# Optimization experiments

Hardware: AMD Instinct MI355X
Metric: run time of the kernel (lower is better)

## Reference

```python
import jax, jax.numpy as jnp
import numpy as np

NUM_NODES = 100000
NUM_EDGES = 1600000
NUM_GRAPHS = 512
HIDDEN = 128
LAYERS = 3
NUM_CLASSES = 10
BN_EPS = 1e-5


def setup_inputs() -> dict:
    key = jax.random.key(0)
    ks = jax.random.split(key, 12)
    x = jax.random.normal(ks[0], (NUM_NODES, HIDDEN), dtype=jnp.float32)
    edge_index = jax.random.randint(ks[1], (2, NUM_EDGES), 0, NUM_NODES, dtype=jnp.int32)
    batch = jnp.sort(jax.random.randint(ks[2], (NUM_NODES,), 0, NUM_GRAPHS, dtype=jnp.int32))
    s = 1.0 / np.sqrt(HIDDEN)
    W1 = jax.random.normal(ks[3], (LAYERS, HIDDEN, HIDDEN), dtype=jnp.float32) * s
    b1 = jnp.zeros((LAYERS, HIDDEN), dtype=jnp.float32)
    W2 = jax.random.normal(ks[4], (LAYERS, HIDDEN, HIDDEN), dtype=jnp.float32) * s
    b2 = jnp.zeros((LAYERS, HIDDEN), dtype=jnp.float32)
    gamma = jnp.ones((LAYERS, HIDDEN), dtype=jnp.float32)
    beta = jnp.zeros((LAYERS, HIDDEN), dtype=jnp.float32)
    eps_gin = jnp.zeros((LAYERS,), dtype=jnp.float32)  # train_eps init 0
    lin1_w = jax.random.normal(ks[5], (LAYERS * HIDDEN, HIDDEN), dtype=jnp.float32) * (1.0 / np.sqrt(LAYERS * HIDDEN))
    lin1_b = jnp.zeros((HIDDEN,), dtype=jnp.float32)
    lin2_w = jax.random.normal(ks[6], (HIDDEN, NUM_CLASSES), dtype=jnp.float32) * s
    lin2_b = jnp.zeros((NUM_CLASSES,), dtype=jnp.float32)
    return {"x": x, "edge_index": edge_index, "batch": batch,
            "W1": W1, "b1": b1, "W2": W2, "b2": b2,
            "gamma": gamma, "beta": beta, "eps_gin": eps_gin,
            "lin1_w": lin1_w, "lin1_b": lin1_b, "lin2_w": lin2_w, "lin2_b": lin2_b}


def _batchnorm(h, g, b):
    mu = jnp.mean(h, axis=0, keepdims=True)
    var = jnp.var(h, axis=0, keepdims=True)
    return (h - mu) * jax.lax.rsqrt(var + BN_EPS) * g + b


def reference(x, edge_index, batch, W1, b1, W2, b2, gamma, beta, eps_gin,
              lin1_w, lin1_b, lin2_w, lin2_b):
    src, dst = edge_index[0], edge_index[1]
    n = x.shape[0]
    h = x
    layer_hs = []
    for l in range(LAYERS):
        # scatter-add neighbor aggregation: agg[i] = sum_{j->i} h[j]
        agg = jax.ops.segment_sum(h[src], dst, num_segments=n)
        z = (1.0 + eps_gin[l]) * h + agg
        z = jax.nn.relu(z @ W1[l] + b1[l])
        z = jax.nn.relu(z @ W2[l] + b2[l])
        h = _batchnorm(z, gamma[l], beta[l])
        layer_hs.append(h)
    h_cat = jnp.concatenate(layer_hs, axis=-1)  # [N, LAYERS*HIDDEN]
    # global mean pool per graph
    sums = jax.ops.segment_sum(h_cat, batch, num_segments=NUM_GRAPHS)
    counts = jax.ops.segment_sum(jnp.ones((n, 1), h_cat.dtype), batch, num_segments=NUM_GRAPHS)
    g = sums / jnp.maximum(counts, 1.0)
    g = jax.nn.relu(g @ lin1_w + lin1_b)
    # dropout is identity in inference
    return g @ lin2_w + lin2_b
```

## Files before the change

### kernel.cpp

```cpp
#include <hip/hip_runtime.h>

#define HID 128
#define NGRAPH 512
#define NLAYERS 3
#define BN_EPS 1e-5f
#define NPB 256
#define EB 4096

typedef __attribute__((ext_vector_type(8))) short bf16x8;
typedef __attribute__((ext_vector_type(4))) float f32x4;
typedef __attribute__((ext_vector_type(2))) float f32x2;

__device__ inline unsigned short f2bf(float x) {
    union { float f; unsigned u; } v; v.f = x;
    unsigned r = v.u + 0x7FFFu + ((v.u >> 16) & 1u);
    return (unsigned short)(r >> 16);
}
__device__ inline float bf2f(unsigned short b) {
    union { float f; unsigned u; } v; v.u = ((unsigned)b) << 16; return v.f;
}
__device__ inline f32x2 bfp(unsigned u) {
    union { unsigned q; float f; } lo, hi;
    lo.q = u << 16; hi.q = u & 0xFFFF0000u;
    f32x2 r; r[0] = lo.f; r[1] = hi.f; return r;
}

__global__ void k_prep(const float4* __restrict__ x4, ushort* __restrict__ xb, int total4,
                       const float* __restrict__ W1, ushort* __restrict__ w1h, ushort* __restrict__ w1l,
                       const float* __restrict__ W2, ushort* __restrict__ w2h, ushort* __restrict__ w2l,
                       int wtotal, int xblocks,
                       const int* __restrict__ dst, int E, int* __restrict__ blkcnt,
                       int* __restrict__ btot) {
    __shared__ int hist[512];
    int b = blockIdx.x, t = threadIdx.x;
    if (b < 384) {
        int gid = b * 256 + t;
        const float* W; ushort *Wh, *Wl; int e;
        if (gid < wtotal) { W = W1; Wh = w1h; Wl = w1l; e = gid; }
        else              { W = W2; Wh = w2h; Wl = w2l; e = gid - wtotal; }
        if (e < wtotal) {
            int l = e >> 14, rem = e & 16383, k = rem >> 7, n = rem & 127;
            float v = W[e];
            ushort hi = f2bf(v);
            ushort lo = f2bf(v - bf2f(hi));
            int o = (l << 14) + (n << 7) + k;
            Wh[o] = hi; Wl[o] = lo;
        }
    } else if (b < 384 + xblocks) {
        int i = (b - 384) * 256 + t;
        if (i < total4) {
            float4 v = x4[i];
            uint2 p;
            p.x = ((unsigned)f2bf(v.y) << 16) | f2bf(v.x);
            p.y = ((unsigned)f2bf(v.w) << 16) | f2bf(v.z);
            ((uint2*)xb)[i] = p;
        }
    } else {
        int b2 = b - (384 + xblocks);
        hist[t] = 0; hist[t + 256] = 0;
        __syncthreads();
        int base = b2 * EB;
        #pragma unroll
        for (int i = 0; i < 16; ++i) {
            int e = base + i * 256 + t;
            if (e < E) atomicAdd(&hist[dst[e] >> 8], 1);
        }
        __syncthreads();
        blkcnt[b2 * 512 + t]       = hist[t];
        blkcnt[b2 * 512 + t + 256] = hist[t + 256];
        if (hist[t])       atomicAdd(&btot[t], hist[t]);
        if (hist[t + 256]) atomicAdd(&btot[t + 256], hist[t + 256]);
    }
}

__global__ __launch_bounds__(512) void k_bscan(const int* __restrict__ tot, int nb, int E,
                                               int* __restrict__ bbase, int* __restrict__ rowptrN) {
    __shared__ int sh[512];
    int t = threadIdx.x;
    sh[t] = (t < nb) ? tot[t] : 0;
    __syncthreads();
    #pragma unroll
    for (int s = 1; s < 512; s <<= 1) {
        int v = (t >= s) ? sh[t - s] : 0;
        __syncthreads();
        sh[t] += v;
        __syncthreads();
    }
    if (t < nb) bbase[t] = (t == 0) ? 0 : sh[t - 1];
    if (t == 0) { bbase[nb] = E; *rowptrN = E; }
}

__global__ __launch_bounds__(512) void k_colscan(int* __restrict__ blkcnt, int eblk,
                                                 const int* __restrict__ bbase) {
    __shared__ int sh[512];
    int t = threadIdx.x;
    int b = blockIdx.x;
    sh[t] = (t < eblk) ? blkcnt[t * 512 + b] : 0;
    __syncthreads();
    #pragma unroll
    for (int s = 1; s < 512; s <<= 1) {
        int v = (t >= s) ? sh[t - s] : 0;
        __syncthreads();
        sh[t] += v;
        __syncthreads();
    }
    int excl = (t == 0) ? 0 : sh[t - 1];
    if (t < eblk) blkcnt[t * 512 + b] = bbase[b] + excl;
}

__global__ __launch_bounds__(256) void k_bscatter(const int* __restrict__ src,
                                                  const int* __restrict__ dst, int E,
                                                  const int* __restrict__ blkcnt,
                                                  unsigned* __restrict__ pairs) {
    __shared__ int hist[512];
    __shared__ int lbase[512];
    int t = threadIdx.x;
    hist[t] = 0; hist[t + 256] = 0;
    lbase[t]       = blkcnt[blockIdx.x * 512 + t];
    lbase[t + 256] = blkcnt[blockIdx.x * 512 + t + 256];
    __syncthreads();
    int base = blockIdx.x * EB;
    #pragma unroll
    for (int i = 0; i < 16; ++i) {
        int e = base + i * 256 + t;
        if (e < E) {
            int d = dst[e];
            int b = d >> 8;
            int pos = lbase[b] + atomicAdd(&hist[b], 1);
            pairs[pos] = ((unsigned)(d & 255) << 24) | (unsigned)src[e];
        }
    }
}

__global__ __launch_bounds__(256) void k_bbuild(const unsigned* __restrict__ pairs,
                                                const int* __restrict__ bbase, int N,
                                                int* __restrict__ rowptr, int* __restrict__ csr) {
    __shared__ int cnt[256];
    __shared__ int off[256];
    int t = threadIdx.x;
    int b = blockIdx.x;
    int base = bbase[b], bcount = bbase[b + 1] - base;
    cnt[t] = 0;
    __syncthreads();
    for (int i = t; i < bcount; i += 256) atomicAdd(&cnt[pairs[base + i] >> 24], 1);
    __syncthreads();
    off[t] = cnt[t];
    __syncthreads();
    for (int s = 1; s < 256; s <<= 1) {
        int v = (t >= s) ? off[t - s] : 0;
        __syncthreads();
        off[t] += v;
        __syncthreads();
    }
    int excl = (t == 0) ? 0 : off[t - 1];
    int node = b * NPB + t;
    if (node < N) rowptr[node] = base + excl;
    cnt[t] = excl;
    __syncthreads();
    for (int i = t; i < bcount; i += 256) {
        unsigned p = pairs[base + i];
        int dl = p >> 24;
        int pos = base + atomicAdd(&cnt[dl], 1);
        csr[pos] = (int)(p & 0xFFFFFFu);
    }
}

__global__ __launch_bounds__(256, 6) void k_agg(
        const int* __restrict__ rowptr, const int* __restrict__ csr_src,
        const uint2* __restrict__ hinb,
        const float* __restrict__ prev_sliced,
        const float* __restrict__ g_row, const float* __restrict__ be_row,
        const float* __restrict__ eps_gin, int layer,
        ushort* __restrict__ z0out, int N) {
    __shared__ float sfold[256];
    const int t = threadIdx.x;
    const int lane = t & 63;
    const int wv = t >> 6;
    const int q = lane >> 4;
    const int f = lane & 15;

    if (prev_sliced) {
        float s = 0.f;
        #pragma unroll
        for (int k = 0; k < 8; ++k) s += prev_sliced[k * 768 + t];
        sfold[t] = s;
        __syncthreads();
    }

    f32x2 scv2[4], shv2[4];
    if (prev_sliced) {
        float invn = 1.0f / (float)N;
        #pragma unroll
        for (int d = 0; d < 4; ++d) {
            #pragma unroll
            for (int h = 0; h < 2; ++h) {
                int fi = f * 8 + d * 2 + h;
                float mu = sfold[fi] * invn;
                float var = sfold[128 + fi] * invn - mu * mu;
                float inv = rsqrtf(var + BN_EPS);
                float scj = g_row[fi] * inv;
                scv2[d][h] = scj; shv2[d][h] = be_row[fi] - mu * scj;
            }
        }
    } else {
        #pragma unroll
        for (int d = 0; d < 4; ++d) { scv2[d] = (f32x2){1.f, 1.f}; shv2[d] = (f32x2){0.f, 0.f}; }
    }
    float e1 = 1.0f + eps_gin[layer];
    const uint4* hin4 = (const uint4*)hinb;

    int r = blockIdx.x * 16 + wv * 4 + q;
    f32x2 a2[4];
    #pragma unroll
    for (int d = 0; d < 4; ++d) a2[d] = (f32x2){0.f, 0.f};
    float cdeg = 0.f;
    if (r < N) {
        int beg = rowptr[r], end = rowptr[r + 1];
        uint4 hv = hin4[(size_t)r * 16 + f];
        a2[0] = e1 * bfp(hv.x); a2[1] = e1 * bfp(hv.y);
        a2[2] = e1 * bfp(hv.z); a2[3] = e1 * bfp(hv.w);
        int p = beg;
        for (; p + 8 <= end; p += 8) {
            int s0 = csr_src[p],     s1 = csr_src[p + 1], s2 = csr_src[p + 2], s3 = csr_src[p + 3];
            int s4 = csr_src[p + 4], s5 = csr_src[p + 5], s6 = csr_src[p + 6], s7 = csr_src[p + 7];
            uint4 v0 = hin4[(size_t)s0 * 16 + f];
            uint4 v1 = hin4[(size_t)s1 * 16 + f];
            uint4 v2 = hin4[(size_t)s2 * 16 + f];
            uint4 v3 = hin4[(size_t)s3 * 16 + f];
            uint4 v4 = hin4[(size_t)s4 * 16 + f];
            uint4 v5 = hin4[(size_t)s5 * 16 + f];
            uint4 v6 = hin4[(size_t)s6 * 16 + f];
            uint4 v7 = hin4[(size_t)s7 * 16 + f];
            a2[0] += ((bfp(v0.x) + bfp(v1.x)) + (bfp(v2.x) + bfp(v3.x)))
                   + ((bfp(v4.x) + bfp(v5.x)) + (bfp(v6.x) + bfp(v7.x)));
            a2[1] += ((bfp(v0.y) + bfp(v1.y)) + (bfp(v2.y) + bfp(v3.y)))
                   + ((bfp(v4.y) + bfp(v5.y)) + (bfp(v6.y) + bfp(v7.y)));
            a2[2] += ((bfp(v0.z) + bfp(v1.z)) + (bfp(v2.z) + bfp(v3.z)))
                   + ((bfp(v4.z) + bfp(v5.z)) + (bfp(v6.z) + bfp(v7.z)));
            a2[3] += ((bfp(v0.w) + bfp(v1.w)) + (bfp(v2.w) + bfp(v3.w)))
                   + ((bfp(v4.w) + bfp(v5.w)) + (bfp(v6.w) + bfp(v7.w)));
        }
        if (p < end) {
            int last = end - 1;
            int c1 = min(p + 1, last), c2 = min(p + 2, last), c3 = min(p + 3, last);
            int c4 = min(p + 4, last), c5 = min(p + 5, last), c6 = min(p + 6, last);
            int s0 = csr_src[p],  s1 = csr_src[c1], s2 = csr_src[c2], s3 = csr_src[c3];
            int s4 = csr_src[c4], s5 = csr_src[c5], s6 = csr_src[c6];
            uint4 v0 = hin4[(size_t)s0 * 16 + f];
            uint4 v1 = hin4[(size_t)s1 * 16 + f];
            uint4 v2 = hin4[(size_t)s2 * 16 + f];
            uint4 v3 = hin4[(size_t)s3 * 16 + f];
            uint4 v4 = hin4[(size_t)s4 * 16 + f];
            uint4 v5 = hin4[(size_t)s5 * 16 + f];
            uint4 v6 = hin4[(size_t)s6 * 16 + f];
            int rem = end - p;
            unsigned m1 = (rem > 1) ? 0xFFFFFFFFu : 0u;
            unsigned m2 = (rem > 2) ? 0xFFFFFFFFu : 0u;
            unsigned m3 = (rem > 3) ? 0xFFFFFFFFu : 0u;
            unsigned m4 = (rem > 4) ? 0xFFFFFFFFu : 0u;
            unsigned m5 = (rem > 5) ? 0xFFFFFFFFu : 0u;
            unsigned m6 = (rem > 6) ? 0xFFFFFFFFu : 0u;
            a2[0] += ((bfp(v0.x) + bfp(v1.x & m1)) + (bfp(v2.x & m2) + bfp(v3.x & m3)))
                   + ((bfp(v4.x & m4) + bfp(v5.x & m5)) + bfp(v6.x & m6));
            a2[1] += ((bfp(v0.y) + bfp(v1.y & m1)) + (bfp(v2.y & m2) + bfp(v3.y & m3)))
                   + ((bfp(v4.y & m4) + bfp(v5.y & m5)) + bfp(v6.y & m6));
            a2[2] += ((bfp(v0.z) + bfp(v1.z & m1)) + (bfp(v2.z & m2) + bfp(v3.z & m3)))
                   + ((bfp(v4.z & m4) + bfp(v5.z & m5)) + bfp(v6.z & m6));
            a2[3] += ((bfp(v0.w) + bfp(v1.w & m1)) + (bfp(v2.w & m2) + bfp(v3.w & m3)))
                   + ((bfp(v4.w & m4) + bfp(v5.w & m5)) + bfp(v6.w & m6));
        }
        cdeg = e1 + (float)(end - beg);
    }
    f32x2 rr2[4];
    #pragma unroll
    for (int d = 0; d < 4; ++d) rr2[d] = scv2[d] * a2[d] + cdeg * shv2[d];
    uint4 ph;
    ph.x = ((unsigned)f2bf(rr2[0][1]) << 16) | f2bf(rr2[0][0]);
    ph.y = ((unsigned)f2bf(rr2[1][1]) << 16) | f2bf(rr2[1][0]);
    ph.z = ((unsigned)f2bf(rr2[2][1]) << 16) | f2bf(rr2[2][0]);
    ph.w = ((unsigned)f2bf(rr2[3][1]) << 16) | f2bf(rr2[3][0]);
    if (r < N) ((uint4*)z0out)[(size_t)r * 16 + f] = ph;
}

__global__ __launch_bounds__(256, 2) void k_mlp_dense(
        const uint4* __restrict__ z0, int layer, const int* __restrict__ batch,
        const ushort* __restrict__ w1h, const ushort* __restrict__ w1l,
        const float* __restrict__ b1,
        const ushort* __restrict__ w2h, const ushort* __restrict__ w2l,
        const float* __restrict__ b2,
        ushort* __restrict__ Hout, float* __restrict__ stat_sl,
        float* __restrict__ gsum, int N) {
    __shared__ __align__(16) ushort smem[8192];
    const int t = threadIdx.x;
    const int lane = t & 63;
    const int wv = t >> 6;
    const int li = lane & 15;
    const int kq = lane >> 4;
    const int n0 = wv * 32;
    const int row0 = blockIdx.x * 64;
    const int swz = (li & 7) * 4;

    bf16x8 w1hr[8], w1lr[8], w2hr[8], w2lr[8];
    #pragma unroll
    for (int ch = 0; ch < 2; ++ch)
        #pragma unroll
        for (int ks = 0; ks < 2; ++ks)
            #pragma unroll
            for (int nt = 0; nt < 2; ++nt) {
                int i = ch * 4 + ks * 2 + nt;
                size_t wo = (size_t)(n0 + nt * 16 + li) * 128 + (ch * 64 + ks * 32 + kq * 8);
                w1hr[i] = *(const bf16x8*)&w1h[wo];
                w1lr[i] = *(const bf16x8*)&w1l[wo];
                w2hr[i] = *(const bf16x8*)&w2h[wo];
                w2lr[i] = *(const bf16x8*)&w2l[wo];
            }

    {
        const uint4 zz = {0u, 0u, 0u, 0u};
        #pragma unroll
        for (int i = 0; i < 4; ++i) {
            int idx = i * 256 + t;
            int r = idx >> 4, f = idx & 15;
            uint4 v = (row0 + r < N) ? z0[(size_t)(row0 + r) * 16 + f] : zz;
            ((uint4*)smem)[r * 16 + (f ^ (r & 7))] = v;
        }
    }
    __syncthreads();

    f32x4 acc[4][2];
    #pragma unroll
    for (int i = 0; i < 4; ++i) {
        acc[i][0] = (f32x4){0.f, 0.f, 0.f, 0.f};
        acc[i][1] = (f32x4){0.f, 0.f, 0.f, 0.f};
    }

    #pragma unroll
    for (int ch = 0; ch < 2; ++ch) {
        #pragma unroll
        for (int ks = 0; ks < 2; ++ks) {
            int kcol = ch * 8 + ks * 4 + kq;
            #pragma unroll
            for (int mt = 0; mt < 4; ++mt) {
                int r = mt * 16 + li;
                int hw = (r * 16 + (kcol ^ (li & 7))) * 8;
                bf16x8 ah = *(const bf16x8*)&smem[hw];
                #pragma unroll
                for (int nt = 0; nt < 2; ++nt) {
                    int i = ch * 4 + ks * 2 + nt;
                    acc[mt][nt] = __builtin_amdgcn_mfma_f32_16x16x32_bf16(ah, w1hr[i], acc[mt][nt], 0, 0, 0);
                    acc[mt][nt] = __builtin_amdgcn_mfma_f32_16x16x32_bf16(ah, w1lr[i], acc[mt][nt], 0, 0, 0);
                }
            }
        }
    }

    float bz0 = b1[n0 + li], bz1 = b1[n0 + 16 + li];
    __syncthreads();
    #pragma unroll
    for (int mt = 0; mt < 4; ++mt) {
        #pragma unroll
        for (int nt = 0; nt < 2; ++nt) {
            int c = n0 + nt * 16 + li;
            int dk = c >> 1;
            int halfbase = (dk >> 5) * 32;
            int dlow = dk & 31;
            int codd = c & 1;
            float bias = nt ? bz1 : bz0;
            #pragma unroll
            for (int reg = 0; reg < 4; ++reg) {
                int r = mt * 16 + kq * 4 + reg;
                float v = fmaxf(acc[mt][nt][reg] + bias, 0.f);
                int us = (r * 64 + halfbase + (dlow ^ ((r & 7) * 4))) * 2 + codd;
                smem[us] = f2bf(v);
            }
        }
    }
    #pragma unroll
    for (int i = 0; i < 4; ++i) {
        acc[i][0] = (f32x4){0.f, 0.f, 0.f, 0.f};
        acc[i][1] = (f32x4){0.f, 0.f, 0.f, 0.f};
    }
    __syncthreads();

    #pragma unroll
    for (int ch = 0; ch < 2; ++ch) {
        #pragma unroll
        for (int ks = 0; ks < 2; ++ks) {
            int aoff = (ks * 16 + kq * 4) ^ swz;
            #pragma unroll
            for (int mt = 0; mt < 4; ++mt) {
                int idx = ((mt * 16 + li) * 64 + ch * 32 + aoff) * 2;
                bf16x8 ah = *(const bf16x8*)&smem[idx];
                #pragma unroll
                for (int nt = 0; nt < 2; ++nt) {
                    int i = ch * 4 + ks * 2 + nt;
                    acc[mt][nt] = __builtin_amdgcn_mfma_f32_16x16x32_bf16(ah, w2hr[i], acc[mt][nt], 0, 0, 0);
                    acc[mt][nt] = __builtin_amdgcn_mfma_f32_16x16x32_bf16(ah, w2lr[i], acc[mt][nt], 0, 0, 0);
                }
            }
        }
    }

    float bb0 = b2[n0 + li], bb1 = b2[n0 + 16 + li];
    int btr[4][4];
    #pragma unroll
    for (int mt = 0; mt < 4; ++mt)
        #pragma unroll
        for (int reg = 0; reg < 4; ++reg) {
            int grow = row0 + mt * 16 + kq * 4 + reg;
            btr[mt][reg] = (grow < N) ? batch[grow] : -1;
        }
    __syncthreads();
    float s0 = 0.f, q0 = 0.f, s1 = 0.f, q1 = 0.f;
    #pragma unroll
    for (int mt = 0; mt < 4; ++mt) {
        #pragma unroll
        for (int reg = 0; reg < 4; ++reg) {
            int r = mt * 16 + kq * 4 + reg;
            float v0 = fmaxf(acc[mt][0][reg] + bb0, 0.f);
            float v1 = fmaxf(acc[mt][1][reg] + bb1, 0.f);
            smem[r * 128 + n0 + li]      = f2bf(v0);
            smem[r * 128 + n0 + 16 + li] = f2bf(v1);
            if (btr[mt][reg] >= 0) {
                s0 += v0; q0 += v0 * v0; s1 += v1; q1 += v1 * v1;
            }
        }
    }
    __syncthreads();
    {
        int valid = N - row0; if (valid > 64) valid = 64;
        int tot = valid * 16;
        for (int i = t; i < tot; i += 256) {
            int r = i >> 4, c = i & 15;
            ((uint4*)&Hout[(size_t)(row0 + r) * HID])[c] = ((const uint4*)smem)[r * 16 + c];
        }
    }
    s0 += __shfl_xor(s0, 16); s0 += __shfl_xor(s0, 32);
    q0 += __shfl_xor(q0, 16); q0 += __shfl_xor(q0, 32);
    s1 += __shfl_xor(s1, 16); s1 += __shfl_xor(s1, 32);
    q1 += __shfl_xor(q1, 16); q1 += __shfl_xor(q1, 32);
    if (kq == 0) {
        float* ss = stat_sl + (blockIdx.x & 7) * 768;
        unsafeAtomicAdd(&ss[n0 + li], s0);
        unsafeAtomicAdd(&ss[128 + n0 + li], q0);
        unsafeAtomicAdd(&ss[n0 + 16 + li], s1);
        unsafeAtomicAdd(&ss[128 + n0 + 16 + li], q1);
    }
    int lastr = N - 1; if (lastr > row0 + 63) lastr = row0 + 63;
    int g_lo = batch[row0], g_hi = batch[lastr];
    int loff = layer * HID;
    for (int g = g_lo; g <= g_hi; ++g) {
        float p0 = 0.f, p1 = 0.f;
        #pragma unroll
        for (int mt = 0; mt < 4; ++mt)
            #pragma unroll
            for (int reg = 0; reg < 4; ++reg) {
                if (btr[mt][reg] == g) {
                    p0 += fmaxf(acc[mt][0][reg] + bb0, 0.f);
                    p1 += fmaxf(acc[mt][1][reg] + bb1, 0.f);
                }
            }
        p0 += __shfl_xor(p0, 16); p0 += __shfl_xor(p0, 32);
        p1 += __shfl_xor(p1, 16); p1 += __shfl_xor(p1, 32);
        if (kq == 0) {
            unsafeAtomicAdd(&gsum[(size_t)g * 384 + loff + n0 + li], p0);
            unsafeAtomicAdd(&gsum[(size_t)g * 384 + loff + n0 + 16 + li], p1);
        }
    }
}

__global__ __launch_bounds__(128) void k_mlp(const int* __restrict__ batch, int N,
                     const float* __restrict__ gsum, const float* __restrict__ sliced,
                     const float* __restrict__ gamma, const float* __restrict__ beta,
                     const float* __restrict__ w1, const float* __restrict__ b1,
                     const float* __restrict__ w2, const float* __restrict__ b2,
                     float* __restrict__ out) {
    __shared__ float gl[8][384];
    __shared__ float hh[8][128];
    int g0 = blockIdx.x * 8, t = threadIdx.x;
    float invn = 1.0f / (float)N;
    float sc[NLAYERS], sh[NLAYERS];
    #pragma unroll
    for (int l = 0; l < NLAYERS; ++l) {
        float sum_ = 0.f, sq_ = 0.f;
        #pragma unroll
        for (int k = 0; k < 8; ++k) {
            sum_ += sliced[k * 768 + l * 256 + t];
            sq_  += sliced[k * 768 + l * 256 + 128 + t];
        }
        float mu = sum_ * invn;
        float var = sq_ * invn - mu * mu;
        float inv = rsqrtf(var + BN_EPS);
        sc[l] = gamma[l * HID + t] * inv;
        sh[l] = beta[l * HID + t] - mu * sc[l];
    }
    for (int j = 0; j < 8; ++j) {
        int g = g0 + j;
        int start, end;
        { int lo = 0, hi = N; while (lo < hi) { int m = (lo + hi) >> 1; if (batch[m] < g) lo = m + 1; else hi = m; } start = lo; }
        { int lo = start, hi = N; while (lo < hi) { int m = (lo + hi) >> 1; if (batch[m] < g + 1) lo = m + 1; else hi = m; } end = lo; }
        float cnt = (float)(end - start);
        float invc = 1.0f / fmaxf(cnt, 1.0f);
        #pragma unroll
        for (int l = 0; l < NLAYERS; ++l)
            gl[j][l * 128 + t] = (gsum[(size_t)g * 384 + l * 128 + t] * sc[l] + sh[l] * cnt) * invc;
    }
    __syncthreads();
    float acc[8];
    #pragma unroll
    for (int j = 0; j < 8; ++j) acc[j] = b1[t];
    for (int k = 0; k < 384; ++k) {
        float wv = w1[k * HID + t];
        #pragma unroll
        for (int j = 0; j < 8; ++j) acc[j] = fmaf(gl[j][k], wv, acc[j]);
    }
    #pragma unroll
    for (int j = 0; j < 8; ++j) hh[j][t] = fmaxf(acc[j], 0.f);
    __syncthreads();
    if (t < 80) {
        int j = t / 10, o = t % 10;
        float a2 = b2[o];
        for (int k = 0; k < 128; ++k) a2 = fmaf(hh[j][k], w2[k * 10 + o], a2);
        out[(g0 + j) * 10 + o] = a2;
    }
}

extern "C" void kernel_launch(void* const* d_in, const int* in_sizes, int n_in,
                              void* d_out, int out_size, void* d_ws, size_t ws_size,
                              hipStream_t stream) {
    const float* x     = (const float*)d_in[0];
    const int*   ei    = (const int*)d_in[1];
    const int*   batch = (const int*)d_in[2];
    const float* W1    = (const float*)d_in[3];
    const float* b1    = (const float*)d_in[4];
    const float* W2    = (const float*)d_in[5];
    const float* b2    = (const float*)d_in[6];
    const float* gamma = (const float*)d_in[7];
    const float* beta  = (const float*)d_in[8];
    const float* epsg  = (const float*)d_in[9];
    const float* l1w   = (const float*)d_in[10];
    const float* l1b   = (const float*)d_in[11];
    const float* l2w   = (const float*)d_in[12];
    const float* l2b   = (const float*)d_in[13];

    const int N = in_sizes[0] / HID;
    const int E = in_sizes[1] / 2;
    const int* src = ei;
    const int* dst = ei + E;
    const int nb = (N + NPB - 1) / NPB;
    const int eblk = (E + EB - 1) / EB;

    float* w = (float*)d_ws;
    const size_t NF = (size_t)N * HID;
    ushort* xb    = (ushort*)(w + NF);
    ushort* hb[3] = { xb + NF, xb + 2 * NF, xb + 3 * NF };
    ushort* z0buf = xb + 4 * NF;
    float* sliced = w + 4 * NF;
    float* gsum   = sliced + 6144;
    int*   btot   = (int*)(gsum + (size_t)NGRAPH * 384);
    int*   rowptr = btot + 513;
    int*   csr    = rowptr + N + 1;
    int*   bbase  = csr + E;
    ushort* wt  = (ushort*)(((uintptr_t)(bbase + nb + 2) + 15) & ~(uintptr_t)15);
    ushort* w1h = wt;
    ushort* w1l = wt + 49152;
    ushort* w2h = wt + 98304;
    ushort* w2l = wt + 147456;

    unsigned* pairs  = (unsigned*)w;
    int*      blkcnt = (int*)(w + 2 * 1024 * 1024);

    hipMemsetAsync(sliced, 0, (6144 + (size_t)NGRAPH * 384 + 513) * sizeof(float), stream);

    const int total4 = (int)(NF / 4);
    const int xblocks = (total4 + 255) / 256;
    const int prep_blocks = 384 + xblocks + eblk;
    k_prep<<<prep_blocks, 256, 0, stream>>>((const float4*)x, xb, total4,
                                            W1, w1h, w1l, W2, w2h, w2l, NLAYERS * HID * HID,
                                            xblocks, dst, E, blkcnt, btot);

    k_bscan<<<1, 512, 0, stream>>>(btot, nb, E, bbase, rowptr + N);
    k_colscan<<<nb, 512, 0, stream>>>(blkcnt, eblk, bbase);
    k_bscatter<<<eblk, 256, 0, stream>>>(src, dst, E, blkcnt, pairs);
    k_bbuild<<<nb, 256, 0, stream>>>(pairs, bbase, N, rowptr, csr);

    for (int l = 0; l < NLAYERS; ++l) {
        const ushort* hin = (l == 0) ? xb : hb[l - 1];
        const float* psl    = (l == 0) ? nullptr : (sliced + (l - 1) * 256);
        const float* grow_  = gamma + (l == 0 ? 0 : (l - 1)) * HID;
        const float* brow_  = beta  + (l == 0 ? 0 : (l - 1)) * HID;

        k_agg<<<(N + 15) / 16, 256, 0, stream>>>(
            rowptr, csr, (const uint2*)hin, psl, grow_, brow_, epsg, l, z0buf, N);

        k_mlp_dense<<<(N + 63) / 64, 256, 0, stream>>>(
            (const uint4*)z0buf, l, batch,
            w1h + (size_t)l * 16384, w1l + (size_t)l * 16384, b1 + l * HID,
            w2h + (size_t)l * 16384, w2l + (size_t)l * 16384, b2 + l * HID,
            hb[l], sliced + l * 256, gsum, N);
    }

    k_mlp<<<NGRAPH / 8, 128, 0, stream>>>(batch, N, gsum, sliced, gamma, beta,
                                          l1w, l1b, l2w, l2b, (float*)d_out);
}
```

Before: 562.3 us.

## Precompute graph node counts in prep and spread final MLP across one block per graph

Per-graph node counts are now gathered in extra blocks of the prep kernel with shared-memory histograms, so the final head no longer binary-searches the batch array. The final pooled MLP moves from 64 blocks handling 8 graphs each to 512 blocks of 256 threads, one graph per block. Each block splits the K reduction of the first linear layer across two halves and does the second layer with a wave shuffle reduction. This raises parallelism in the small tail kernel, at the cost of re-reading lin1 weights once per graph instead of once per 8 graphs.

```diff
diff --git a/kernel.cpp b/kernel.cpp
--- a/kernel.cpp
+++ b/kernel.cpp
@@ -30,7 +30,8 @@
                        const float* __restrict__ W2, ushort* __restrict__ w2h, ushort* __restrict__ w2l,
                        int wtotal, int xblocks,
                        const int* __restrict__ dst, int E, int* __restrict__ blkcnt,
-                       int* __restrict__ btot) {
+                       int* __restrict__ btot,
+                       const int* __restrict__ batch, int N, int eblk, int* __restrict__ gcnt) {
     __shared__ int hist[512];
     int b = blockIdx.x, t = threadIdx.x;
     if (b < 384) {
@@ -55,7 +56,7 @@
             p.y = ((unsigned)f2bf(v.w) << 16) | f2bf(v.z);
             ((uint2*)xb)[i] = p;
         }
-    } else {
+    } else if (b < 384 + xblocks + eblk) {
         int b2 = b - (384 + xblocks);
         hist[t] = 0; hist[t + 256] = 0;
         __syncthreads();
@@ -70,6 +71,19 @@
         blkcnt[b2 * 512 + t + 256] = hist[t + 256];
         if (hist[t])       atomicAdd(&btot[t], hist[t]);
         if (hist[t + 256]) atomicAdd(&btot[t + 256], hist[t + 256]);
+    } else {
+        int b3 = b - (384 + xblocks + eblk);
+        hist[t] = 0; hist[t + 256] = 0;
+        __syncthreads();
+        int base = b3 * 4096;
+        #pragma unroll
+        for (int i = 0; i < 16; ++i) {
+            int n = base + i * 256 + t;
+            if (n < N) atomicAdd(&hist[batch[n]], 1);
+        }
+        __syncthreads();
+        if (hist[t])       atomicAdd(&gcnt[t], hist[t]);
+        if (hist[t + 256]) atomicAdd(&gcnt[t + 256], hist[t + 256]);
     }
 }
 
@@ -469,59 +483,58 @@
     }
 }
 
-__global__ __launch_bounds__(128) void k_mlp(const int* __restrict__ batch, int N,
+__global__ __launch_bounds__(256) void k_mlp(const int* __restrict__ gcnt, int N,
                      const float* __restrict__ gsum, const float* __restrict__ sliced,
                      const float* __restrict__ gamma, const float* __restrict__ beta,
                      const float* __restrict__ w1, const float* __restrict__ b1,
                      const float* __restrict__ w2, const float* __restrict__ b2,
                      float* __restrict__ out) {
-    __shared__ float gl[8][384];
-    __shared__ float hh[8][128];
-    int g0 = blockIdx.x * 8, t = threadIdx.x;
+    __shared__ float gl[384];
+    __shared__ float ph[2][128];
+    __shared__ float hh[128];
+    int g = blockIdx.x, t = threadIdx.x;
+    float cnt = (float)gcnt[g];
+    float invc = 1.0f / fmaxf(cnt, 1.0f);
     float invn = 1.0f / (float)N;
-    float sc[NLAYERS], sh[NLAYERS];
-    #pragma unroll
-    for (int l = 0; l < NLAYERS; ++l) {
+    for (int i = t; i < 384; i += 256) {
+        int l = i >> 7, f = i & 127;
         float sum_ = 0.f, sq_ = 0.f;
         #pragma unroll
         for (int k = 0; k < 8; ++k) {
-            sum_ += sliced[k * 768 + l * 256 + t];
-            sq_  += sliced[k * 768 + l * 256 + 128 + t];
+            sum_ += sliced[k * 768 + l * 256 + f];
+            sq_  += sliced[k * 768 + l * 256 + 128 + f];
         }
         float mu = sum_ * invn;
         float var = sq_ * invn - mu * mu;
         float inv = rsqrtf(var + BN_EPS);
-        sc[l] = gamma[l * HID + t] * inv;
-        sh[l] = beta[l * HID + t] - mu * sc[l];
-    }
-    for (int j = 0; j < 8; ++j) {
-        int g = g0 + j;
-        int start, end;
-        { int lo = 0, hi = N; while (lo < hi) { int m = (lo + hi) >> 1; if (batch[m] < g) lo = m + 1; else hi = m; } start = lo; }
-        { int lo = start, hi = N; while (lo < hi) { int m = (lo + hi) >> 1; if (batch[m] < g + 1) lo = m + 1; else hi = m; } end = lo; }
-        float cnt = (float)(end - start);
-        float invc = 1.0f / fmaxf(cnt, 1.0f);
-        #pragma unroll
-        for (int l = 0; l < NLAYERS; ++l)
-            gl[j][l * 128 + t] = (gsum[(size_t)g * 384 + l * 128 + t] * sc[l] + sh[l] * cnt) * invc;
-    }
-    __syncthreads();
-    float acc[8];
-    #pragma unroll
-    for (int j = 0; j < 8; ++j) acc[j] = b1[t];
-    for (int k = 0; k < 384; ++k) {
-        float wv = w1[k * HID + t];
-        #pragma unroll
-        for (int j = 0; j < 8; ++j) acc[j] = fmaf(gl[j][k], wv, acc[j]);
-    }
-    #pragma unroll
-    for (int j = 0; j < 8; ++j) hh[j][t] = fmaxf(acc[j], 0.f);
-    __syncthreads();
-    if (t < 80) {
-        int j = t / 10, o = t % 10;
-        float a2 = b2[o];
-        for (int k = 0; k < 128; ++k) a2 = fmaf(hh[j][k], w2[k * 10 + o], a2);
-        out[(g0 + j) * 10 + o] = a2;
+        float sc = gamma[l * HID + f] * inv;
+        float sh = beta[l * HID + f] - mu * sc;
+        gl[i] = (gsum[(size_t)g * 384 + i] * sc + sh * cnt) * invc;
+    }
+    __syncthreads();
+    int f = t & 127, kh = t >> 7;
+    float acc = kh ? 0.f : b1[f];
+    for (int k = kh * 192; k < kh * 192 + 192; ++k)
+        acc = fmaf(gl[k], w1[k * HID + f], acc);
+    ph[kh][f] = acc;
+    __syncthreads();
+    if (t < 128) hh[t] = fmaxf(ph[0][t] + ph[1][t], 0.f);
+    __syncthreads();
+    if (t < 64) {
+        float h0 = hh[t], h1 = hh[t + 64];
+        float p[10];
+        #pragma unroll
+        for (int o = 0; o < 10; ++o)
+            p[o] = h0 * w2[t * 10 + o] + h1 * w2[(t + 64) * 10 + o];
+        #pragma unroll
+        for (int o = 0; o < 10; ++o) {
+            #pragma unroll
+            for (int s = 32; s > 0; s >>= 1) p[o] += __shfl_xor(p[o], s);
+        }
+        if (t == 0) {
+            #pragma unroll
+            for (int o = 0; o < 10; ++o) out[g * 10 + o] = b2[o] + p[o];
+        }
     }
 }
 
@@ -558,7 +571,8 @@
     float* sliced = w + 4 * NF;
     float* gsum   = sliced + 6144;
     int*   btot   = (int*)(gsum + (size_t)NGRAPH * 384);
-    int*   rowptr = btot + 513;
+    int*   gcnt   = btot + 513;
+    int*   rowptr = gcnt + 512;
     int*   csr    = rowptr + N + 1;
     int*   bbase  = csr + E;
     ushort* wt  = (ushort*)(((uintptr_t)(bbase + nb + 2) + 15) & ~(uintptr_t)15);
@@ -570,14 +584,16 @@
     unsigned* pairs  = (unsigned*)w;
     int*      blkcnt = (int*)(w + 2 * 1024 * 1024);
 
-    hipMemsetAsync(sliced, 0, (6144 + (size_t)NGRAPH * 384 + 513) * sizeof(float), stream);
+    hipMemsetAsync(sliced, 0, (6144 + (size_t)NGRAPH * 384 + 513 + 512) * sizeof(float), stream);
 
     const int total4 = (int)(NF / 4);
     const int xblocks = (total4 + 255) / 256;
-    const int prep_blocks = 384 + xblocks + eblk;
+    const int gblocks = (N + 4095) / 4096;
+    const int prep_blocks = 384 + xblocks + eblk + gblocks;
     k_prep<<<prep_blocks, 256, 0, stream>>>((const float4*)x, xb, total4,
                                             W1, w1h, w1l, W2, w2h, w2l, NLAYERS * HID * HID,
-                                            xblocks, dst, E, blkcnt, btot);
+                                            xblocks, dst, E, blkcnt, btot,
+                                            batch, N, eblk, gcnt);
 
     k_bscan<<<1, 512, 0, stream>>>(btot, nb, E, bbase, rowptr + N);
     k_colscan<<<nb, 512, 0, stream>>>(blkcnt, eblk, bbase);
@@ -600,6 +616,6 @@
             hb[l], sliced + l * 256, gsum, N);
     }
 
-    k_mlp<<<NGRAPH / 8, 128, 0, stream>>>(batch, N, gsum, sliced, gamma, beta,
-                                          l1w, l1b, l2w, l2b, (float*)d_out);
-}
+    k_mlp<<<NGRAPH, 256, 0, stream>>>(gcnt, N, gsum, sliced, gamma, beta,
+                                      l1w, l1b, l2w, l2b, (float*)d_out);
+}
```

Result: faster. 517.6 us (-7.9%).
